# Performance work log

Hardware: AMD Instinct MI355X
Metric: run time of the kernel (lower is better)

## Reference

```python
import math
import jax, jax.numpy as jnp
import numpy as np

L, H, D, FF, V, S = 12, 12, 768, 3072, 32000, 1024
HD = D // H
EPS = 1e-5
B, T = 2, 1024


def layernorm(x, w, b):
    mu = jnp.mean(x, axis=-1, keepdims=True)
    var = jnp.mean(jnp.square(x - mu), axis=-1, keepdims=True)
    return (x - mu) * jax.lax.rsqrt(var + EPS) * w + b


def setup_inputs() -> dict:
    key = jax.random.key(0)
    ks = jax.random.split(key, 12)
    std = 0.02
    std_res = 0.02 / math.sqrt(2 * L)  # out_proj / down_proj scaled init
    return {
        "input_ids": jax.random.randint(ks[0], (B, T), 0, V),
        "tok_emb": jax.random.normal(ks[1], (V, D), jnp.float32) * std,
        "pos_emb": jax.random.normal(ks[2], (S, D), jnp.float32) * std,
        "ln1_w": jnp.ones((L, D), jnp.float32),
        "ln1_b": jnp.zeros((L, D), jnp.float32),
        "qkv_w": jax.random.normal(ks[3], (L, 3 * D, D), jnp.float32) * std,
        "out_w": jax.random.normal(ks[4], (L, D, D), jnp.float32) * std_res,
        "ln2_w": jnp.ones((L, D), jnp.float32),
        "ln2_b": jnp.zeros((L, D), jnp.float32),
        "up_w": jax.random.normal(ks[5], (L, FF, D), jnp.float32) * std,
        "down_w": jax.random.normal(ks[6], (L, D, FF), jnp.float32) * std_res,
        "lnf_w": jnp.ones((D,), jnp.float32),
        "lnf_b": jnp.zeros((D,), jnp.float32),
    }


def reference(input_ids, tok_emb, pos_emb, ln1_w, ln1_b, qkv_w, out_w,
              ln2_w, ln2_b, up_w, down_w, lnf_w, lnf_b):
    b, t = input_ids.shape
    x = tok_emb[input_ids] + pos_emb[:t]  # (B,T,D); dropout = eval no-op
    causal = jnp.tril(jnp.ones((t, t), bool))  # (T,T)
    scale = 1.0 / math.sqrt(HD)

    def block(x, p):
        l1w, l1b, qkvw, ow, l2w, l2b, uw, dw = p
        h = layernorm(x, l1w, l1b)
        qkv = h @ qkvw.T  # (B,T,3D)
        q, k, v = jnp.split(qkv, 3, axis=-1)
        q = q.reshape(b, t, H, HD)
        k = k.reshape(b, t, H, HD)
        v = v.reshape(b, t, H, HD)
        scores = jnp.einsum('bihd,bjhd->bhij', q, k) * scale
        scores = jnp.where(causal, scores, -jnp.inf)
        probs = jax.nn.softmax(scores, axis=-1)  # attn_dropout = eval no-op
        o = jnp.einsum('bhij,bjhd->bihd', probs, v).reshape(b, t, D)
        x = x + o @ ow.T
        h2 = layernorm(x, l2w, l2b)
        x = x + jax.nn.gelu(h2 @ uw.T, approximate=False) @ dw.T
        return x, None

    x, _ = jax.lax.scan(block, x, (ln1_w, ln1_b, qkv_w, out_w, ln2_w, ln2_b, up_w, down_w))
    x = layernorm(x, lnf_w, lnf_b)
    logits = x @ tok_emb.T  # tied lm_head
    return logits
```

## Files before the change

kernel.cpp:

```cpp
#include <hip/hip_runtime.h>
#include <hip/hip_bf16.h>
#include <math.h>

#define L_  12
#define H_  12
#define D_  768
#define FF_ 3072
#define V_  32000
#define T_  1024
#define B_  2
#define BT_ (B_*T_)

typedef unsigned short ushort_t;
typedef unsigned int   uint_t;
typedef __bf16 bf16x8 __attribute__((ext_vector_type(8)));
typedef float  f32x4  __attribute__((ext_vector_type(4)));

__device__ __forceinline__ uint_t f2bf1(float f) {
    uint_t u = __builtin_bit_cast(uint_t, f);
    return (u + 0x7FFFu + ((u >> 16) & 1u)) >> 16;
}
__device__ __forceinline__ uint_t f2bf2(float lo, float hi) {
    return f2bf1(lo) | (f2bf1(hi) << 16);
}

__device__ __forceinline__ void gl_lds16(const ushort_t* g, ushort_t* l) {
    __builtin_amdgcn_global_load_lds(
        (const __attribute__((address_space(1))) uint_t*)g,
        (__attribute__((address_space(3))) uint_t*)l, 16, 0, 0);
}

__global__ __launch_bounds__(256) void cast_bf16(const float* __restrict__ in,
                                                 ushort_t* __restrict__ out, int n8)
{
    for (int i = blockIdx.x * 256 + threadIdx.x; i < n8; i += gridDim.x * 256) {
        const float4* p = (const float4*)(in + (size_t)i * 8);
        float4 a = p[0], b = p[1];
        *(uint4*)(out + (size_t)i * 8) =
            make_uint4(f2bf2(a.x,a.y), f2bf2(a.z,a.w), f2bf2(b.x,b.y), f2bf2(b.z,b.w));
    }
}

__global__ __launch_bounds__(256) void cast_layer(const float* __restrict__ q,
    const float* __restrict__ o, const float* __restrict__ u, const float* __restrict__ d,
    ushort_t* __restrict__ out)
{
    const int N0 = 3*D_*D_/8, N1 = N0 + D_*D_/8, N2 = N1 + FF_*D_/8, N3 = N2 + D_*FF_/8;
    for (int i = blockIdx.x * 256 + threadIdx.x; i < N3; i += gridDim.x * 256) {
        const float* src;
        if      (i < N0) src = q + (size_t)i * 8;
        else if (i < N1) src = o + (size_t)(i - N0) * 8;
        else if (i < N2) src = u + (size_t)(i - N1) * 8;
        else             src = d + (size_t)(i - N2) * 8;
        const float4* p = (const float4*)src;
        float4 a = p[0], b = p[1];
        *(uint4*)(out + (size_t)i * 8) =
            make_uint4(f2bf2(a.x,a.y), f2bf2(a.z,a.w), f2bf2(b.x,b.y), f2bf2(b.z,b.w));
    }
}

#define EPI_F32   0
#define EPI_BF16  1
#define EPI_GELU  2
#define EPI_ATOM  3

template <int EPI>
__global__ __launch_bounds__(256) void gemm_bt(
    const ushort_t* __restrict__ A, const ushort_t* __restrict__ W,
    void* __restrict__ Cv, int N, int K, int MT, int KS, int Kc)
{
    __shared__ ushort_t As[128 * 32];
    __shared__ ushort_t Bs[128 * 32];

    const int tid  = threadIdx.x;
    const int w    = tid >> 6;
    const int lane = tid & 63;

    const int nwg = gridDim.x;
    int swz = (blockIdx.x & 7) * (nwg >> 3) + (blockIdx.x >> 3);
    const int mt   = swz % MT;
    int rest       = swz / MT;
    const int ks   = rest % KS;
    const int nt   = rest / KS;
    const int m0 = mt * 128, n0 = nt * 128;
    const int kb = ks * Kc,  ke = kb + Kc;

    const int srow = lane >> 2;
    const int scol = (lane & 3) * 8;
    const ushort_t* gA = A + (size_t)(m0 + w * 32 + srow) * K + scol;
    const ushort_t* gW = W + (size_t)(n0 + w * 32 + srow) * K + scol;
    ushort_t* lA = As + w * 1024;
    ushort_t* lB = Bs + w * 1024;
    const size_t row16 = (size_t)16 * K;

    const int lr = lane & 15;
    const int lk = (lane >> 4) * 8;
    const int wm = (w >> 1) * 64;
    const int wn = (w & 1) * 64;

    f32x4 acc[4][4] = {};

    for (int k0 = kb; k0 < ke; k0 += 32) {
        gl_lds16(gA + k0,         lA);
        gl_lds16(gA + k0 + row16, lA + 512);
        gl_lds16(gW + k0,         lB);
        gl_lds16(gW + k0 + row16, lB + 512);
        __syncthreads();

        bf16x8 av[4], bv[4];
        #pragma unroll
        for (int i = 0; i < 4; ++i)
            av[i] = *(const bf16x8*)&As[(wm + i * 16 + lr) * 32 + lk];
        #pragma unroll
        for (int j = 0; j < 4; ++j)
            bv[j] = *(const bf16x8*)&Bs[(wn + j * 16 + lr) * 32 + lk];
        #pragma unroll
        for (int i = 0; i < 4; ++i)
            #pragma unroll
            for (int j = 0; j < 4; ++j)
                acc[i][j] = __builtin_amdgcn_mfma_f32_16x16x32_bf16(av[i], bv[j], acc[i][j], 0, 0, 0);
        __syncthreads();
    }

    float*    Cf = (float*)Cv;
    ushort_t* Cb = (ushort_t*)Cv;
    const int rbase = (lane >> 4) * 4;
    #pragma unroll
    for (int i = 0; i < 4; ++i) {
        #pragma unroll
        for (int j = 0; j < 4; ++j) {
            #pragma unroll
            for (int r = 0; r < 4; ++r) {
                int row = m0 + wm + i * 16 + rbase + r;
                int col = n0 + wn + j * 16 + lr;
                size_t idx = (size_t)row * N + col;
                float v = acc[i][j][r];
                if (EPI == EPI_F32)  Cf[idx] = v;
                if (EPI == EPI_BF16) Cb[idx] = (ushort_t)f2bf1(v);
                if (EPI == EPI_GELU) Cb[idx] = (ushort_t)f2bf1(0.5f * v * (1.0f + erff(v * 0.70710678118654752f)));
                if (EPI == EPI_ATOM) atomicAdd(&Cf[idx], v);
            }
        }
    }
}

__global__ __launch_bounds__(256) void vprep(const ushort_t* __restrict__ qkv,
                                             ushort_t* __restrict__ vt)
{
    __shared__ ushort_t Vs[64][72];
    const int blk   = blockIdx.x;
    const int ttile = blk & 15;
    const int bh    = blk >> 4;
    const int b     = bh / H_;
    const int h     = bh % H_;
    const int tid   = threadIdx.x;
    const int t0    = ttile * 64;
    {
        const int tr = tid >> 2;
        const int dc = (tid & 3) * 16;
        const uint4* src = (const uint4*)(qkv + (size_t)(b * T_ + t0 + tr) * 2304 + 1536 + h * 64 + dc);
        uint4 v0 = src[0], v1 = src[1];
        *(uint4*)&Vs[tr][dc]     = v0;
        *(uint4*)&Vs[tr][dc + 8] = v1;
    }
    __syncthreads();
    {
        const int d  = tid >> 2;
        const int jc = (tid & 3) * 16;
        uint_t w[8];
        #pragma unroll
        for (int i = 0; i < 8; ++i)
            w[i] = (uint_t)Vs[jc + 2*i][d] | ((uint_t)Vs[jc + 2*i + 1][d] << 16);
        uint4* dst = (uint4*)(vt + ((size_t)bh * 64 + d) * T_ + t0 + jc);
        dst[0] = make_uint4(w[0], w[1], w[2], w[3]);
        dst[1] = make_uint4(w[4], w[5], w[6], w[7]);
    }
}

__global__ __launch_bounds__(256) void attn_mfma(const ushort_t* __restrict__ qkv,
    const ushort_t* __restrict__ vt, ushort_t* __restrict__ o)
{
    __shared__ ushort_t Ks[64 * 72];
    __shared__ ushort_t Vts[64 * 72];
    __shared__ ushort_t Ps[4][16 * 72];

    const int bid = blockIdx.x;
    const int qt  = 15 - (bid & 15);
    const int bh  = bid >> 4;
    const int b   = bh / H_;
    const int h   = bh % H_;
    const int tid  = threadIdx.x;
    const int wq   = tid >> 6;
    const int lane = tid & 63;
    const int l15  = lane & 15;
    const int lg   = lane >> 4;
    const int qbase = qt * 64;

    bf16x8 qf0, qf1;
    {
        const ushort_t* qp = qkv + (size_t)(b * T_ + qbase + wq * 16 + l15) * 2304 + h * 64 + lg * 8;
        qf0 = *(const bf16x8*)qp;
        qf1 = *(const bf16x8*)(qp + 32);
    }

    f32x4 od[4] = {};
    float mr[4] = {-INFINITY, -INFINITY, -INFINITY, -INFINITY};
    float lr[4] = {0.f, 0.f, 0.f, 0.f};

    const int tr = tid >> 2;
    const int cb = (tid & 3) * 16;
    const ushort_t* kgp = qkv + (size_t)(b * T_ + tr) * 2304 + 768 + h * 64 + cb;
    const ushort_t* vgp = vt + ((size_t)bh * 64 + tr) * T_ + cb;

    for (int jt = 0; jt <= qt; ++jt) {
        {
            const uint4* ks = (const uint4*)(kgp + (size_t)jt * 64 * 2304);
            uint4 k0 = ks[0], k1 = ks[1];
            const uint4* vs = (const uint4*)(vgp + jt * 64);
            uint4 v0 = vs[0], v1 = vs[1];
            *(uint4*)&Ks[tr * 72 + cb]      = k0;
            *(uint4*)&Ks[tr * 72 + cb + 8]  = k1;
            *(uint4*)&Vts[tr * 72 + cb]     = v0;
            *(uint4*)&Vts[tr * 72 + cb + 8] = v1;
        }
        __syncthreads();

        f32x4 s[4];
        #pragma unroll
        for (int n = 0; n < 4; ++n) {
            const ushort_t* kr = &Ks[(16 * n + l15) * 72 + lg * 8];
            bf16x8 kf0 = *(const bf16x8*)kr;
            bf16x8 kf1 = *(const bf16x8*)(kr + 32);
            f32x4 a = {};
            a = __builtin_amdgcn_mfma_f32_16x16x32_bf16(qf0, kf0, a, 0, 0, 0);
            a = __builtin_amdgcn_mfma_f32_16x16x32_bf16(qf1, kf1, a, 0, 0, 0);
            s[n] = a;
        }

        const bool diag = (jt == qt);
        #pragma unroll
        for (int n = 0; n < 4; ++n) {
            #pragma unroll
            for (int r = 0; r < 4; ++r) {
                float v = s[n][r] * 0.125f;
                if (diag) {
                    int jg = 16 * n + l15;
                    int qg = wq * 16 + lg * 4 + r;
                    if (jg > qg) v = -INFINITY;
                }
                s[n][r] = v;
            }
        }

        float al[4];
        #pragma unroll
        for (int r = 0; r < 4; ++r) {
            float tm = fmaxf(fmaxf(s[0][r], s[1][r]), fmaxf(s[2][r], s[3][r]));
            tm = fmaxf(tm, __shfl_xor(tm, 1, 64));
            tm = fmaxf(tm, __shfl_xor(tm, 2, 64));
            tm = fmaxf(tm, __shfl_xor(tm, 4, 64));
            tm = fmaxf(tm, __shfl_xor(tm, 8, 64));
            float mn = fmaxf(mr[r], tm);
            al[r] = __expf(mr[r] - mn);
            mr[r] = mn;
        }
        #pragma unroll
        for (int n = 0; n < 4; ++n)
            #pragma unroll
            for (int r = 0; r < 4; ++r)
                s[n][r] = __expf(s[n][r] - mr[r]);
        #pragma unroll
        for (int r = 0; r < 4; ++r) {
            float ps = s[0][r] + s[1][r] + s[2][r] + s[3][r];
            ps += __shfl_xor(ps, 1, 64);
            ps += __shfl_xor(ps, 2, 64);
            ps += __shfl_xor(ps, 4, 64);
            ps += __shfl_xor(ps, 8, 64);
            lr[r] = lr[r] * al[r] + ps;
        }
        #pragma unroll
        for (int n = 0; n < 4; ++n)
            #pragma unroll
            for (int r = 0; r < 4; ++r)
                od[n][r] *= al[r];

        #pragma unroll
        for (int n = 0; n < 4; ++n)
            #pragma unroll
            for (int r = 0; r < 4; ++r)
                Ps[wq][(lg * 4 + r) * 72 + 16 * n + l15] = (ushort_t)f2bf1(s[n][r]);

        #pragma unroll
        for (int kc = 0; kc < 2; ++kc) {
            bf16x8 pa = *(const bf16x8*)&Ps[wq][l15 * 72 + kc * 32 + lg * 8];
            #pragma unroll
            for (int n = 0; n < 4; ++n) {
                bf16x8 vf = *(const bf16x8*)&Vts[(16 * n + l15) * 72 + kc * 32 + lg * 8];
                od[n] = __builtin_amdgcn_mfma_f32_16x16x32_bf16(pa, vf, od[n], 0, 0, 0);
            }
        }
        __syncthreads();
    }

    #pragma unroll
    for (int r = 0; r < 4; ++r) {
        float inv = 1.0f / lr[r];
        int row = qbase + wq * 16 + lg * 4 + r;
        ushort_t* op = o + ((size_t)(b * T_ + row)) * 768 + h * 64 + l15;
        #pragma unroll
        for (int n = 0; n < 4; ++n)
            op[16 * n] = (ushort_t)f2bf1(od[n][r] * inv);
    }
}

__global__ __launch_bounds__(256) void ln_kernel(const float* __restrict__ x,
    const float* __restrict__ w, const float* __restrict__ bia, ushort_t* __restrict__ out)
{
    const int row = blockIdx.x;
    const int tid = threadIdx.x;
    const float* xr = x + (size_t)row * 768;
    float v0 = xr[tid], v1 = xr[tid + 256], v2 = xr[tid + 512];
    float s  = v0 + v1 + v2;
    float s2 = v0 * v0 + v1 * v1 + v2 * v2;
    #pragma unroll
    for (int off = 32; off > 0; off >>= 1) {
        s  += __shfl_down(s,  off, 64);
        s2 += __shfl_down(s2, off, 64);
    }
    __shared__ float sh[8];
    const int wave = tid >> 6;
    if ((tid & 63) == 0) { sh[wave] = s; sh[4 + wave] = s2; }
    __syncthreads();
    float S  = sh[0] + sh[1] + sh[2] + sh[3];
    float S2 = sh[4] + sh[5] + sh[6] + sh[7];
    float mean = S * (1.f / 768.f);
    float var  = S2 * (1.f / 768.f) - mean * mean;
    float inv  = rsqrtf(var + 1e-5f);
    ushort_t* orow = out + (size_t)row * 768;
    orow[tid]       = (ushort_t)f2bf1((v0 - mean) * inv * w[tid]       + bia[tid]);
    orow[tid + 256] = (ushort_t)f2bf1((v1 - mean) * inv * w[tid + 256] + bia[tid + 256]);
    orow[tid + 512] = (ushort_t)f2bf1((v2 - mean) * inv * w[tid + 512] + bia[tid + 512]);
}

__global__ __launch_bounds__(256) void embed_kernel(const int* __restrict__ ids,
    const float* __restrict__ tok, const float* __restrict__ pos, float* __restrict__ x)
{
    const int bt = blockIdx.x;
    const int t  = bt % T_;
    const int id = ids[bt];
    const int tid = threadIdx.x;
    const float* tr = tok + (size_t)id * 768;
    const float* pr = pos + (size_t)t * 768;
    float* xr = x + (size_t)bt * 768;
    xr[tid]       = tr[tid]       + pr[tid];
    xr[tid + 256] = tr[tid + 256] + pr[tid + 256];
    xr[tid + 512] = tr[tid + 512] + pr[tid + 512];
}

extern "C" void kernel_launch(void* const* d_in, const int* in_sizes, int n_in,
                              void* d_out, int out_size, void* d_ws, size_t ws_size,
                              hipStream_t stream)
{
    const int*   ids   = (const int*)  d_in[0];
    const float* tok   = (const float*)d_in[1];
    const float* pos   = (const float*)d_in[2];
    const float* ln1w  = (const float*)d_in[3];
    const float* ln1b  = (const float*)d_in[4];
    const float* qkvw  = (const float*)d_in[5];
    const float* outw  = (const float*)d_in[6];
    const float* ln2w  = (const float*)d_in[7];
    const float* ln2b  = (const float*)d_in[8];
    const float* upw   = (const float*)d_in[9];
    const float* downw = (const float*)d_in[10];
    const float* lnfw  = (const float*)d_in[11];
    const float* lnfb  = (const float*)d_in[12];
    float* out = (float*)d_out;

    char* ws = (char*)d_ws;
    ushort_t* h    = (ushort_t*)ws;
    float*    x    = (float*)   (ws + 3145728);
    ushort_t* qkv  = (ushort_t*)(ws + 9437184);
    ushort_t* o    = qkv  + (size_t)BT_ * 3 * D_;
    ushort_t* vt   = o    + (size_t)BT_ * D_;
    ushort_t* ffh  = vt   + (size_t)B_ * H_ * 64 * T_;
    ushort_t* layerW = ffh + (size_t)BT_ * FF_;
    ushort_t* tokW = (ushort_t*)(ws + 3145728);

    ushort_t* qkvwB  = layerW;
    ushort_t* outwB  = qkvwB + (size_t)3 * D_ * D_;
    ushort_t* upwB   = outwB + (size_t)D_ * D_;
    ushort_t* downwB = upwB  + (size_t)FF_ * D_;

    embed_kernel<<<BT_, 256, 0, stream>>>(ids, tok, pos, x);

    for (int l = 0; l < L_; ++l) {
        cast_layer<<<1024, 256, 0, stream>>>(
            qkvw  + (size_t)l * 3 * D_ * D_,
            outw  + (size_t)l * D_ * D_,
            upw   + (size_t)l * FF_ * D_,
            downw + (size_t)l * D_ * FF_, layerW);

        ln_kernel<<<BT_, 256, 0, stream>>>(x, ln1w + l * D_, ln1b + l * D_, h);

        gemm_bt<EPI_BF16><<<16 * (3 * D_ / 128), 256, 0, stream>>>(
            h, qkvwB, qkv, 3 * D_, D_, 16, 1, D_);

        vprep<<<B_ * H_ * (T_ / 64), 256, 0, stream>>>(qkv, vt);
        attn_mfma<<<B_ * H_ * (T_ / 64), 256, 0, stream>>>(qkv, vt, o);

        gemm_bt<EPI_ATOM><<<16 * (D_ / 128) * 2, 256, 0, stream>>>(
            o, outwB, x, D_, D_, 16, 2, D_ / 2);

        ln_kernel<<<BT_, 256, 0, stream>>>(x, ln2w + l * D_, ln2b + l * D_, h);

        gemm_bt<EPI_GELU><<<16 * (FF_ / 128), 256, 0, stream>>>(
            h, upwB, ffh, FF_, D_, 16, 1, D_);

        gemm_bt<EPI_ATOM><<<16 * (D_ / 128) * 4, 256, 0, stream>>>(
            ffh, downwB, x, D_, FF_, 16, 4, FF_ / 4);
    }

    ln_kernel<<<BT_, 256, 0, stream>>>(x, lnfw, lnfb, h);
    cast_bf16<<<2048, 256, 0, stream>>>(tok, tokW, V_ * D_ / 8);
    gemm_bt<EPI_F32><<<16 * (V_ / 128), 256, 0, stream>>>(
        h, tokW, out, V_, D_, 16, 1, D_);
}
```

Baseline: 2.211 ms.

## Double GEMM K-tile with XOR-swizzled LDS and rewrite attention as single-wave blocks

The GEMM now stages 64-wide K tiles instead of 32, with an XOR swizzle on LDS chunk addresses to avoid bank conflicts, and turns the M-tile and split-K counts into compile-time constants. Attention switches from 4-wave 64-query blocks to single-wave 16-query blocks that process 128 keys per step. These blocks read K and V straight from global memory with no shared staging or barriers, use exp2 with a folded log2e scale, and raise wave priority around the MFMA sections. The goals are fewer barriers per K step, less LDS contention and finer causal load balancing. The cost is more global/L2 traffic for K and V, because tiles are no longer shared across waves.

```diff
diff --git a/kernel.cpp b/kernel.cpp
--- a/kernel.cpp
+++ b/kernel.cpp
@@ -64,13 +64,13 @@
 #define EPI_GELU  2
 #define EPI_ATOM  3
 
-template <int EPI>
+template <int EPI, int KS>
 __global__ __launch_bounds__(256) void gemm_bt(
     const ushort_t* __restrict__ A, const ushort_t* __restrict__ W,
-    void* __restrict__ Cv, int N, int K, int MT, int KS, int Kc)
-{
-    __shared__ ushort_t As[128 * 32];
-    __shared__ ushort_t Bs[128 * 32];
+    void* __restrict__ Cv, int N, int K, int Kc)
+{
+    __shared__ ushort_t As[128 * 64];
+    __shared__ ushort_t Bs[128 * 64];
 
     const int tid  = threadIdx.x;
     const int w    = tid >> 6;
@@ -78,47 +78,57 @@
 
     const int nwg = gridDim.x;
     int swz = (blockIdx.x & 7) * (nwg >> 3) + (blockIdx.x >> 3);
-    const int mt   = swz % MT;
-    int rest       = swz / MT;
-    const int ks   = rest % KS;
+    const int mt   = swz & 15;
+    int rest       = swz >> 4;
+    const int ks   = rest & (KS - 1);
     const int nt   = rest / KS;
     const int m0 = mt * 128, n0 = nt * 128;
     const int kb = ks * Kc,  ke = kb + Kc;
 
-    const int srow = lane >> 2;
-    const int scol = (lane & 3) * 8;
+    const int srow = lane >> 3;
+    const int scol = ((lane & 7) ^ srow) * 8;
     const ushort_t* gA = A + (size_t)(m0 + w * 32 + srow) * K + scol;
     const ushort_t* gW = W + (size_t)(n0 + w * 32 + srow) * K + scol;
-    ushort_t* lA = As + w * 1024;
-    ushort_t* lB = Bs + w * 1024;
-    const size_t row16 = (size_t)16 * K;
+    ushort_t* lA = As + w * 2048;
+    ushort_t* lB = Bs + w * 2048;
+    const size_t row8 = (size_t)8 * K;
 
     const int lr = lane & 15;
-    const int lk = (lane >> 4) * 8;
+    const int lg = lane >> 4;
     const int wm = (w >> 1) * 64;
     const int wn = (w & 1) * 64;
 
     f32x4 acc[4][4] = {};
 
-    for (int k0 = kb; k0 < ke; k0 += 32) {
-        gl_lds16(gA + k0,         lA);
-        gl_lds16(gA + k0 + row16, lA + 512);
-        gl_lds16(gW + k0,         lB);
-        gl_lds16(gW + k0 + row16, lB + 512);
+    for (int k0 = kb; k0 < ke; k0 += 64) {
+        #pragma unroll
+        for (int i = 0; i < 4; ++i) {
+            gl_lds16(gA + k0 + i * row8, lA + i * 512);
+            gl_lds16(gW + k0 + i * row8, lB + i * 512);
+        }
         __syncthreads();
 
-        bf16x8 av[4], bv[4];
-        #pragma unroll
-        for (int i = 0; i < 4; ++i)
-            av[i] = *(const bf16x8*)&As[(wm + i * 16 + lr) * 32 + lk];
-        #pragma unroll
-        for (int j = 0; j < 4; ++j)
-            bv[j] = *(const bf16x8*)&Bs[(wn + j * 16 + lr) * 32 + lk];
-        #pragma unroll
-        for (int i = 0; i < 4; ++i)
-            #pragma unroll
-            for (int j = 0; j < 4; ++j)
-                acc[i][j] = __builtin_amdgcn_mfma_f32_16x16x32_bf16(av[i], bv[j], acc[i][j], 0, 0, 0);
+        #pragma unroll
+        for (int kk = 0; kk < 2; ++kk) {
+            bf16x8 av[4], bv[4];
+            #pragma unroll
+            for (int i = 0; i < 4; ++i) {
+                int rr = wm + i * 16 + lr;
+                int ch = (lg + 4 * kk) ^ (rr & 7);
+                av[i] = *(const bf16x8*)&As[rr * 64 + ch * 8];
+            }
+            #pragma unroll
+            for (int j = 0; j < 4; ++j) {
+                int rr = wn + j * 16 + lr;
+                int ch = (lg + 4 * kk) ^ (rr & 7);
+                bv[j] = *(const bf16x8*)&Bs[rr * 64 + ch * 8];
+            }
+            #pragma unroll
+            for (int i = 0; i < 4; ++i)
+                #pragma unroll
+                for (int j = 0; j < 4; ++j)
+                    acc[i][j] = __builtin_amdgcn_mfma_f32_16x16x32_bf16(av[i], bv[j], acc[i][j], 0, 0, 0);
+        }
         __syncthreads();
     }
 
@@ -177,77 +187,61 @@
     }
 }
 
-__global__ __launch_bounds__(256) void attn_mfma(const ushort_t* __restrict__ qkv,
+__global__ __launch_bounds__(64) void attn_mfma(const ushort_t* __restrict__ qkv,
     const ushort_t* __restrict__ vt, ushort_t* __restrict__ o)
 {
-    __shared__ ushort_t Ks[64 * 72];
-    __shared__ ushort_t Vts[64 * 72];
-    __shared__ ushort_t Ps[4][16 * 72];
-
-    const int bid = blockIdx.x;
-    const int qt  = 15 - (bid & 15);
-    const int bh  = bid >> 4;
+    __shared__ ushort_t Ps[16 * 136];
+
+    int swz = (blockIdx.x & 7) * 192 + (blockIdx.x >> 3);
+    const int bh  = swz >> 6;
+    const int qtl = 63 - (swz & 63);
     const int b   = bh / H_;
     const int h   = bh % H_;
-    const int tid  = threadIdx.x;
-    const int wq   = tid >> 6;
-    const int lane = tid & 63;
+    const int lane = threadIdx.x;
     const int l15  = lane & 15;
     const int lg   = lane >> 4;
-    const int qbase = qt * 64;
-
-    bf16x8 qf0, qf1;
-    {
-        const ushort_t* qp = qkv + (size_t)(b * T_ + qbase + wq * 16 + l15) * 2304 + h * 64 + lg * 8;
-        qf0 = *(const bf16x8*)qp;
-        qf1 = *(const bf16x8*)(qp + 32);
-    }
+    const int qbase = qtl * 16;
+    const int qlast = qbase + 15;
+
+    const ushort_t* qp = qkv + ((size_t)(b * T_) + qbase + l15) * 2304 + h * 64 + lg * 8;
+    bf16x8 qf0 = *(const bf16x8*)qp;
+    bf16x8 qf1 = *(const bf16x8*)(qp + 32);
 
     f32x4 od[4] = {};
     float mr[4] = {-INFINITY, -INFINITY, -INFINITY, -INFINITY};
     float lr[4] = {0.f, 0.f, 0.f, 0.f};
 
-    const int tr = tid >> 2;
-    const int cb = (tid & 3) * 16;
-    const ushort_t* kgp = qkv + (size_t)(b * T_ + tr) * 2304 + 768 + h * 64 + cb;
-    const ushort_t* vgp = vt + ((size_t)bh * 64 + tr) * T_ + cb;
-
-    for (int jt = 0; jt <= qt; ++jt) {
-        {
-            const uint4* ks = (const uint4*)(kgp + (size_t)jt * 64 * 2304);
-            uint4 k0 = ks[0], k1 = ks[1];
-            const uint4* vs = (const uint4*)(vgp + jt * 64);
-            uint4 v0 = vs[0], v1 = vs[1];
-            *(uint4*)&Ks[tr * 72 + cb]      = k0;
-            *(uint4*)&Ks[tr * 72 + cb + 8]  = k1;
-            *(uint4*)&Vts[tr * 72 + cb]     = v0;
-            *(uint4*)&Vts[tr * 72 + cb + 8] = v1;
-        }
-        __syncthreads();
-
-        f32x4 s[4];
-        #pragma unroll
-        for (int n = 0; n < 4; ++n) {
-            const ushort_t* kr = &Ks[(16 * n + l15) * 72 + lg * 8];
-            bf16x8 kf0 = *(const bf16x8*)kr;
-            bf16x8 kf1 = *(const bf16x8*)(kr + 32);
-            f32x4 a = {};
-            a = __builtin_amdgcn_mfma_f32_16x16x32_bf16(qf0, kf0, a, 0, 0, 0);
-            a = __builtin_amdgcn_mfma_f32_16x16x32_bf16(qf1, kf1, a, 0, 0, 0);
-            s[n] = a;
-        }
-
-        const bool diag = (jt == qt);
-        #pragma unroll
-        for (int n = 0; n < 4; ++n) {
+    const ushort_t* kbase = qkv + (size_t)(b * T_) * 2304 + 768 + h * 64;
+    const ushort_t* vbase = vt + (size_t)bh * 64 * T_;
+    const float SC = 0.18033688011112042f;
+
+    for (int j0 = 0; j0 <= qlast; j0 += 128) {
+        f32x4 s[8];
+        __builtin_amdgcn_s_setprio(1);
+        #pragma unroll
+        for (int n = 0; n < 8; ++n) {
+            if (j0 + 16 * n <= qlast) {
+                const ushort_t* kr = kbase + (size_t)(j0 + 16 * n + l15) * 2304 + lg * 8;
+                bf16x8 kf0 = *(const bf16x8*)kr;
+                bf16x8 kf1 = *(const bf16x8*)(kr + 32);
+                f32x4 a = {};
+                a = __builtin_amdgcn_mfma_f32_16x16x32_bf16(qf0, kf0, a, 0, 0, 0);
+                a = __builtin_amdgcn_mfma_f32_16x16x32_bf16(qf1, kf1, a, 0, 0, 0);
+                s[n] = a;
+            } else {
+                s[n] = f32x4{-INFINITY, -INFINITY, -INFINITY, -INFINITY};
+            }
+        }
+        __builtin_amdgcn_s_setprio(0);
+
+        #pragma unroll
+        for (int n = 0; n < 8; ++n) {
             #pragma unroll
             for (int r = 0; r < 4; ++r) {
-                float v = s[n][r] * 0.125f;
-                if (diag) {
-                    int jg = 16 * n + l15;
-                    int qg = wq * 16 + lg * 4 + r;
-                    if (jg > qg) v = -INFINITY;
-                }
+                float v = s[n][r] * SC;
+                int jg = j0 + 16 * n + l15;
+                int qg = qbase + lg * 4 + r;
+                if (jg > qg) v = -INFINITY;
                 s[n][r] = v;
             }
         }
@@ -255,23 +249,25 @@
         float al[4];
         #pragma unroll
         for (int r = 0; r < 4; ++r) {
-            float tm = fmaxf(fmaxf(s[0][r], s[1][r]), fmaxf(s[2][r], s[3][r]));
+            float tm = fmaxf(fmaxf(fmaxf(s[0][r], s[1][r]), fmaxf(s[2][r], s[3][r])),
+                             fmaxf(fmaxf(s[4][r], s[5][r]), fmaxf(s[6][r], s[7][r])));
             tm = fmaxf(tm, __shfl_xor(tm, 1, 64));
             tm = fmaxf(tm, __shfl_xor(tm, 2, 64));
             tm = fmaxf(tm, __shfl_xor(tm, 4, 64));
             tm = fmaxf(tm, __shfl_xor(tm, 8, 64));
             float mn = fmaxf(mr[r], tm);
-            al[r] = __expf(mr[r] - mn);
+            al[r] = exp2f(mr[r] - mn);
             mr[r] = mn;
         }
         #pragma unroll
-        for (int n = 0; n < 4; ++n)
+        for (int n = 0; n < 8; ++n)
             #pragma unroll
             for (int r = 0; r < 4; ++r)
-                s[n][r] = __expf(s[n][r] - mr[r]);
+                s[n][r] = exp2f(s[n][r] - mr[r]);
         #pragma unroll
         for (int r = 0; r < 4; ++r) {
-            float ps = s[0][r] + s[1][r] + s[2][r] + s[3][r];
+            float ps = (s[0][r] + s[1][r]) + (s[2][r] + s[3][r]);
+            ps += (s[4][r] + s[5][r]) + (s[6][r] + s[7][r]);
             ps += __shfl_xor(ps, 1, 64);
             ps += __shfl_xor(ps, 2, 64);
             ps += __shfl_xor(ps, 4, 64);
@@ -285,31 +281,34 @@
                 od[n][r] *= al[r];
 
         #pragma unroll
-        for (int n = 0; n < 4; ++n)
+        for (int n = 0; n < 8; ++n)
             #pragma unroll
             for (int r = 0; r < 4; ++r)
-                Ps[wq][(lg * 4 + r) * 72 + 16 * n + l15] = (ushort_t)f2bf1(s[n][r]);
-
-        #pragma unroll
-        for (int kc = 0; kc < 2; ++kc) {
-            bf16x8 pa = *(const bf16x8*)&Ps[wq][l15 * 72 + kc * 32 + lg * 8];
-            #pragma unroll
-            for (int n = 0; n < 4; ++n) {
-                bf16x8 vf = *(const bf16x8*)&Vts[(16 * n + l15) * 72 + kc * 32 + lg * 8];
-                od[n] = __builtin_amdgcn_mfma_f32_16x16x32_bf16(pa, vf, od[n], 0, 0, 0);
-            }
-        }
-        __syncthreads();
+                Ps[(lg * 4 + r) * 136 + 16 * n + l15] = (ushort_t)f2bf1(s[n][r]);
+
+        __builtin_amdgcn_s_setprio(1);
+        #pragma unroll
+        for (int kc = 0; kc < 4; ++kc) {
+            if (j0 + kc * 32 <= qlast) {
+                bf16x8 pa = *(const bf16x8*)&Ps[l15 * 136 + kc * 32 + lg * 8];
+                #pragma unroll
+                for (int nn = 0; nn < 4; ++nn) {
+                    bf16x8 vf = *(const bf16x8*)&vbase[(size_t)(16 * nn + l15) * T_ + j0 + kc * 32 + lg * 8];
+                    od[nn] = __builtin_amdgcn_mfma_f32_16x16x32_bf16(pa, vf, od[nn], 0, 0, 0);
+                }
+            }
+        }
+        __builtin_amdgcn_s_setprio(0);
     }
 
     #pragma unroll
     for (int r = 0; r < 4; ++r) {
         float inv = 1.0f / lr[r];
-        int row = qbase + wq * 16 + lg * 4 + r;
+        int row = qbase + lg * 4 + r;
         ushort_t* op = o + ((size_t)(b * T_ + row)) * 768 + h * 64 + l15;
         #pragma unroll
-        for (int n = 0; n < 4; ++n)
-            op[16 * n] = (ushort_t)f2bf1(od[n][r] * inv);
+        for (int nn = 0; nn < 4; ++nn)
+            op[16 * nn] = (ushort_t)f2bf1(od[nn][r] * inv);
     }
 }
 
@@ -402,26 +401,26 @@
 
         ln_kernel<<<BT_, 256, 0, stream>>>(x, ln1w + l * D_, ln1b + l * D_, h);
 
-        gemm_bt<EPI_BF16><<<16 * (3 * D_ / 128), 256, 0, stream>>>(
-            h, qkvwB, qkv, 3 * D_, D_, 16, 1, D_);
+        gemm_bt<EPI_BF16, 1><<<16 * (3 * D_ / 128), 256, 0, stream>>>(
+            h, qkvwB, qkv, 3 * D_, D_, D_);
 
         vprep<<<B_ * H_ * (T_ / 64), 256, 0, stream>>>(qkv, vt);
-        attn_mfma<<<B_ * H_ * (T_ / 64), 256, 0, stream>>>(qkv, vt, o);
-
-        gemm_bt<EPI_ATOM><<<16 * (D_ / 128) * 2, 256, 0, stream>>>(
-            o, outwB, x, D_, D_, 16, 2, D_ / 2);
+        attn_mfma<<<B_ * H_ * (T_ / 16), 64, 0, stream>>>(qkv, vt, o);
+
+        gemm_bt<EPI_ATOM, 2><<<16 * (D_ / 128) * 2, 256, 0, stream>>>(
+            o, outwB, x, D_, D_, D_ / 2);
 
         ln_kernel<<<BT_, 256, 0, stream>>>(x, ln2w + l * D_, ln2b + l * D_, h);
 
-        gemm_bt<EPI_GELU><<<16 * (FF_ / 128), 256, 0, stream>>>(
-            h, upwB, ffh, FF_, D_, 16, 1, D_);
-
-        gemm_bt<EPI_ATOM><<<16 * (D_ / 128) * 4, 256, 0, stream>>>(
-            ffh, downwB, x, D_, FF_, 16, 4, FF_ / 4);
+        gemm_bt<EPI_GELU, 1><<<16 * (FF_ / 128), 256, 0, stream>>>(
+            h, upwB, ffh, FF_, D_, D_);
+
+        gemm_bt<EPI_ATOM, 4><<<16 * (D_ / 128) * 4, 256, 0, stream>>>(
+            ffh, downwB, x, D_, FF_, FF_ / 4);
     }
 
     ln_kernel<<<BT_, 256, 0, stream>>>(x, lnfw, lnfb, h);
     cast_bf16<<<2048, 256, 0, stream>>>(tok, tokW, V_ * D_ / 8);
-    gemm_bt<EPI_F32><<<16 * (V_ / 128), 256, 0, stream>>>(
-        h, tokW, out, V_, D_, 16, 1, D_);
-}
+    gemm_bt<EPI_F32, 1><<<16 * (V_ / 128), 256, 0, stream>>>(
+        h, tokW, out, V_, D_, D_);
+}
```

Result: no change. 2.195 ms (-0.7%).
